# Kernel optimization log

Measured on AMD Instinct MI355X. Metric: run time of the kernel, lower is better.

## Reference

```python
import jax, jax.numpy as jnp
import numpy as np

DIM = 512
HEADS = 8
DIM_HEAD = 64
LANDMARKS = 256  # dim // 2
PINV_ITERS = 6
KERNEL = 33  # residual conv kernel
NUM_LAYERS = 2
NUM_CLASSES = 2


def layernorm(x, g, b, eps=1e-5):
    mu = x.mean(-1, keepdims=True)
    var = ((x - mu) ** 2).mean(-1, keepdims=True)
    return (x - mu) * jax.lax.rsqrt(var + eps) * g + b


def moore_penrose_pinv(x, iters=PINV_ITERS):
    # x: (b, h, m, m); scaling uses GLOBAL max over all batch/heads (torch.max)
    abs_x = jnp.abs(x)
    col = abs_x.sum(-1).max()
    row = abs_x.sum(-2).max()
    z = jnp.swapaxes(x, -1, -2) / (col * row)
    I = jnp.eye(x.shape[-1], dtype=x.dtype)
    for _ in range(iters):
        xz = x @ z
        z = 0.25 * z @ (13. * I - xz @ (15. * I - xz @ (7. * I - xz)))
    return z


def nystrom_attention(x, w_qkv, w_out, b_out, conv_w):
    # x: (b, n, dim)
    b, n, _ = x.shape
    m = LANDMARKS
    pad = (m - n % m) % m
    if pad:
        x = jnp.pad(x, ((0, 0), (pad, 0), (0, 0)))  # pad at FRONT
    nf = n + pad
    qkv = x @ w_qkv  # (b, nf, 3*h*dh)
    qkv = qkv.reshape(b, nf, 3, HEADS, DIM_HEAD)
    q = jnp.transpose(qkv[:, :, 0], (0, 2, 1, 3)) * (DIM_HEAD ** -0.5)  # (b,h,nf,dh)
    k = jnp.transpose(qkv[:, :, 1], (0, 2, 1, 3))
    v = jnp.transpose(qkv[:, :, 2], (0, 2, 1, 3))
    l = nf // m
    q_l = q.reshape(b, HEADS, m, l, DIM_HEAD).mean(3)  # (b,h,m,dh)
    k_l = k.reshape(b, HEADS, m, l, DIM_HEAD).mean(3)
    sim1 = jnp.einsum('bhid,bhjd->bhij', q, k_l)      # (b,h,nf,m)
    sim2 = jnp.einsum('bhid,bhjd->bhij', q_l, k_l)    # (b,h,m,m)
    sim3 = jnp.einsum('bhid,bhjd->bhij', q_l, k)      # (b,h,m,nf)
    attn1 = jax.nn.softmax(sim1, axis=-1)
    attn2 = jax.nn.softmax(sim2, axis=-1)
    attn3 = jax.nn.softmax(sim3, axis=-1)
    attn2_inv = moore_penrose_pinv(attn2)
    out = (attn1 @ attn2_inv) @ (attn3 @ v)  # (b,h,nf,dh)
    # residual depthwise conv over sequence dim, per head (Conv2d groups=heads)
    res = jax.lax.conv_general_dilated(
        v, conv_w, window_strides=(1, 1), padding=((KERNEL // 2, KERNEL // 2), (0, 0)),
        dimension_numbers=('NCHW', 'OIHW', 'NCHW'), feature_group_count=HEADS)
    out = out + res
    out = jnp.transpose(out, (0, 2, 1, 3)).reshape(b, nf, HEADS * DIM_HEAD)
    out = out @ w_out + b_out
    return out[:, -n:]


def setup_inputs() -> dict:
    key = jax.random.key(0)
    ks = jax.random.split(key, 16)
    B, N = 2, 8191
    s = 0.02
    inp = {
        'h': jax.random.normal(ks[0], (B, N, 1024), jnp.float32),
        'w1': jax.random.normal(ks[1], (1024, DIM), jnp.float32) * s,
        'b1': jnp.zeros((DIM,), jnp.float32),
        'cls_token': jax.random.normal(ks[2], (1, 1, DIM), jnp.float32),
        'ln_g': jnp.ones((NUM_LAYERS, DIM), jnp.float32),
        'ln_b': jnp.zeros((NUM_LAYERS, DIM), jnp.float32),
        'w_qkv': jax.random.normal(ks[3], (NUM_LAYERS, DIM, 3 * HEADS * DIM_HEAD), jnp.float32) * s,
        'w_out': jax.random.normal(ks[4], (NUM_LAYERS, HEADS * DIM_HEAD, DIM), jnp.float32) * s,
        'b_out': jnp.zeros((NUM_LAYERS, DIM), jnp.float32),
        'conv_w': jax.random.normal(ks[5], (NUM_LAYERS, HEADS, 1, KERNEL, 1), jnp.float32) * s,
        'fn_g': jnp.ones((DIM,), jnp.float32),
        'fn_b': jnp.zeros((DIM,), jnp.float32),
        'w2': jax.random.normal(ks[6], (DIM, NUM_CLASSES), jnp.float32) * s,
        'b2': jnp.zeros((NUM_CLASSES,), jnp.float32),
    }
    return inp


def reference(h, w1, b1, cls_token, ln_g, ln_b, w_qkv, w_out, b_out, conv_w, fn_g, fn_b, w2, b2):
    x = jax.nn.relu(h @ w1 + b1)  # (B,N,512)
    B = x.shape[0]
    cls = jnp.broadcast_to(cls_token, (B, 1, DIM))
    x = jnp.concatenate([cls, x], axis=1)  # (B, N+1, 512)
    for i in range(NUM_LAYERS):
        x = x + nystrom_attention(layernorm(x, ln_g[i], ln_b[i]), w_qkv[i], w_out[i], b_out[i], conv_w[i])
    x = layernorm(x, fn_g, fn_b)[:, 0]
    logits = x @ w2 + b2
    return logits
```

## Files before the change

kernel.cpp:

```cpp
#include <hip/hip_runtime.h>
#include <hip/hip_bf16.h>

#define DIM 512
#define HEADS 8
#define DH 64
#define LM 256
#define NF 8192
#define BHN 16

typedef __attribute__((ext_vector_type(8))) short short8;
typedef __attribute__((ext_vector_type(4))) float f32x4;

__device__ __forceinline__ float bf2f(unsigned short u) {
  return __uint_as_float((unsigned)u << 16);
}
__device__ __forceinline__ unsigned short f2bf(float x) {
  unsigned u = __float_as_uint(x);
  unsigned r = u + 0x7fffu + ((u >> 16) & 1u);
  return (unsigned short)(r >> 16);
}

__device__ __forceinline__ void gl2lds16(const void* g, void* l) {
  __builtin_amdgcn_global_load_lds(
      (const __attribute__((address_space(1))) void*)g,
      (__attribute__((address_space(3))) void*)l, 16, 0, 0);
}

__device__ __forceinline__ float waveReduceSum(float v) {
#pragma unroll
  for (int o = 1; o < 64; o <<= 1) v += __shfl_xor(v, o);
  return v;
}
__device__ __forceinline__ float waveReduceMax(float v) {
#pragma unroll
  for (int o = 1; o < 64; o <<= 1) v = fmaxf(v, __shfl_xor(v, o));
  return v;
}
__device__ __forceinline__ float blockReduceSum256(float v, float* sm) {
  v = waveReduceSum(v);
  int w = threadIdx.x >> 6;
  __syncthreads();
  if ((threadIdx.x & 63) == 0) sm[w] = v;
  __syncthreads();
  return sm[0] + sm[1] + sm[2] + sm[3];
}
__device__ __forceinline__ float blockReduceMax256(float v, float* sm) {
  v = waveReduceMax(v);
  int w = threadIdx.x >> 6;
  __syncthreads();
  if ((threadIdx.x & 63) == 0) sm[w] = v;
  __syncthreads();
  return fmaxf(fmaxf(sm[0], sm[1]), fmaxf(sm[2], sm[3]));
}

__global__ __launch_bounds__(256)
void cvt_bf16(const float* __restrict__ in, unsigned short* __restrict__ out,
              long long n) {
  long long i = ((long long)blockIdx.x * 256 + threadIdx.x) * 4;
  if (i + 3 < n) {
    float4 v = *(const float4*)&in[i];
    ushort4 o;
    o.x = f2bf(v.x); o.y = f2bf(v.y); o.z = f2bf(v.z); o.w = f2bf(v.w);
    *(ushort4*)&out[i] = o;
  } else {
    for (; i < n; i++) out[i] = f2bf(in[i]);
  }
}

__global__ __launch_bounds__(256)
void cvt_transpose(const float* __restrict__ in, unsigned short* __restrict__ out,
                   int Kd, int Nd) {
  __shared__ float t[32][33];
  int x = threadIdx.x & 31, y = threadIdx.x >> 5;
#pragma unroll
  for (int i = 0; i < 32; i += 8) {
    int k = blockIdx.y * 32 + y + i, n = blockIdx.x * 32 + x;
    t[y + i][x] = in[(long long)k * Nd + n];
  }
  __syncthreads();
#pragma unroll
  for (int i = 0; i < 32; i += 8) {
    int n = blockIdx.x * 32 + y + i, k = blockIdx.y * 32 + x;
    out[(long long)n * Kd + k] = f2bf(t[x][y + i]);
  }
}

__global__ __launch_bounds__(256)
void vt_transpose(const unsigned short* __restrict__ VB,
                  unsigned short* __restrict__ VT) {
  __shared__ unsigned short t[64][80];
  int bh = blockIdx.x >> 7, tile = blockIdx.x & 127;
  int n0 = tile * 64;
  int tid = threadIdx.x;
#pragma unroll
  for (int it = 0; it < 2; it++) {
    int s = it * 256 + tid;
    int nl = s >> 3, sg = s & 7;
    *(short8*)&t[nl][sg * 8] =
        *(const short8*)&VB[((long long)bh * NF + n0 + nl) * DH + sg * 8];
  }
  __syncthreads();
#pragma unroll
  for (int it = 0; it < 2; it++) {
    int s = it * 256 + tid;
    int dl = s >> 3, sg = s & 7;
    short8 v;
#pragma unroll
    for (int j = 0; j < 8; j++) ((unsigned short*)&v)[j] = t[sg * 8 + j][dl];
    *(short8*)&VT[((long long)bh * DH + dl) * NF + n0 + sg * 8] = v;
  }
}

__global__ __launch_bounds__(256) void zero_f(float* __restrict__ p, int n) {
  int i = blockIdx.x * 256 + threadIdx.x;
  if (i < n) p[i] = 0.f;
}

__global__ __launch_bounds__(256) void write_cls(const float* __restrict__ cls,
                                                 float* __restrict__ X) {
  int t = blockIdx.x * 256 + threadIdx.x;
  int b = t >> 9, c = t & 511;
  X[(long long)b * NF * DIM + c] = cls[c];
}

#define MG_RELU 1
#define MG_ADDC 2
#define MG_BIAS 4
__global__ __launch_bounds__(256)
void gemm_mfma(const unsigned short* __restrict__ A,
               const unsigned short* __restrict__ B,
               const float* __restrict__ bias, float* __restrict__ C,
               unsigned short* __restrict__ qkv, unsigned short* __restrict__ vbuf,
               int M, int N, int K, int flags, int remap) {
  __shared__ short8 smem[1024];
  short8 (*Als)[64] = (short8 (*)[64])smem;
  short8 (*Bls)[64] = (short8 (*)[64])(smem + 512);
  const int tid = threadIdx.x;
  const int lane = tid & 63, wave = tid >> 6;
  const int wm = wave >> 1, wn = wave & 1;
  const int m0 = blockIdx.y * 128, n0 = blockIdx.x * 128;
  const int r16 = lane & 15, quad = lane >> 4;
  const unsigned short* pa0 = A + (long long)(m0 + 32 * wave + r16) * K + quad * 8;
  const unsigned short* pa1 = A + (long long)(m0 + 32 * wave + 16 + r16) * K + quad * 8;
  const unsigned short* pb0 = B + (long long)(n0 + 32 * wave + r16) * K + quad * 8;
  const unsigned short* pb1 = B + (long long)(n0 + 32 * wave + 16 + r16) * K + quad * 8;
  f32x4 acc[4][4] = {};
  for (int k0 = 0; k0 < K; k0 += 32) {
    gl2lds16(pa0, &Als[2 * wave][0]);
    gl2lds16(pa1, &Als[2 * wave + 1][0]);
    gl2lds16(pb0, &Bls[2 * wave][0]);
    gl2lds16(pb1, &Bls[2 * wave + 1][0]);
    pa0 += 32; pa1 += 32; pb0 += 32; pb1 += 32;
    __syncthreads();
    short8 af[4], bfr[4];
#pragma unroll
    for (int mt = 0; mt < 4; mt++) af[mt] = Als[wm * 4 + mt][lane];
#pragma unroll
    for (int nt = 0; nt < 4; nt++) bfr[nt] = Bls[wn * 4 + nt][lane];
#pragma unroll
    for (int mt = 0; mt < 4; mt++)
#pragma unroll
      for (int nt = 0; nt < 4; nt++)
        acc[mt][nt] = __builtin_amdgcn_mfma_f32_16x16x32_bf16(
            af[mt], bfr[nt], acc[mt][nt], 0, 0, 0);
    __syncthreads();
  }
  if (remap == 2) {
    unsigned short (*Ep)[32][64] = (unsigned short (*)[32][64])smem;
    int gn_base = n0 + wn * 64;
    int s = gn_base >> 9, hh = (gn_base >> 6) & 7;
    float scale = (s == 0) ? 0.125f : 1.f;
    unsigned short* basep =
        (s == 0) ? qkv : (s == 1) ? qkv + (long long)BHN * NF * DH : vbuf;
#pragma unroll
    for (int half = 0; half < 2; half++) {
      __builtin_amdgcn_s_waitcnt(0);
#pragma unroll
      for (int mt = half * 2; mt < half * 2 + 2; mt++)
#pragma unroll
        for (int nt = 0; nt < 4; nt++)
#pragma unroll
          for (int r = 0; r < 4; r++)
            Ep[wave][(mt & 1) * 16 + quad * 4 + r][nt * 16 + r16] =
                f2bf(acc[mt][nt][r] * scale);
      __builtin_amdgcn_s_waitcnt(0);
#pragma unroll
      for (int it = 0; it < 4; it++) {
        int idx = it * 64 + lane;
        int m_l = idx >> 3, sg = idx & 7;
        int gm = m0 + wm * 64 + half * 32 + m_l;
        int b = gm >> 13, n = gm & (NF - 1);
        int bh = b * HEADS + hh;
        short8 v = *(short8*)&Ep[wave][m_l][sg * 8];
        *(short8*)&basep[((long long)bh * NF + n) * DH + sg * 8] = v;
      }
    }
  } else {
#pragma unroll
    for (int mt = 0; mt < 4; mt++) {
#pragma unroll
      for (int nt = 0; nt < 4; nt++) {
#pragma unroll
        for (int r = 0; r < 4; r++) {
          int gm = m0 + wm * 64 + mt * 16 + quad * 4 + r;
          int gn = n0 + wn * 64 + nt * 16 + r16;
          if (gm >= M) continue;
          float v = acc[mt][nt][r];
          if (flags & MG_BIAS) v += bias[gn];
          long long idx;
          if (remap == 1) {
            int b = gm / 8191;
            int n = gm - b * 8191;
            idx = ((long long)(b * NF + 1 + n)) * DIM + gn;
          } else {
            idx = (long long)gm * N + gn;
          }
          if (flags & MG_ADDC) v += C[idx];
          if (flags & MG_RELU) v = fmaxf(v, 0.f);
          C[idx] = v;
        }
      }
    }
  }
}

__global__ __launch_bounds__(256)
void flash_attn1(const unsigned short* __restrict__ QB,
                 const unsigned short* __restrict__ KLB,
                 const unsigned short* __restrict__ WmB,
                 const unsigned short* __restrict__ XNC,
                 unsigned short* __restrict__ XNB2) {
  __shared__ unsigned short Plds[4][16][136];
  const int bh = blockIdx.y, b = bh >> 3, hh = bh & 7;
  const int tid = threadIdx.x, lane = tid & 63, wave = tid >> 6;
  const int r16 = lane & 15, quad = lane >> 4;
  const int m0w = blockIdx.x * 64 + wave * 16;
  const unsigned short* Aq = QB + (long long)bh * NF * DH;
  const unsigned short* Bk = KLB + (long long)bh * LM * DH;
  short8 af[2];
#pragma unroll
  for (int kc = 0; kc < 2; kc++)
    af[kc] = *(const short8*)&Aq[(long long)(m0w + r16) * DH + kc * 32 + quad * 8];
  f32x4 S[16] = {};
  __builtin_amdgcn_s_setprio(1);
#pragma unroll
  for (int nt = 0; nt < 16; nt++) {
#pragma unroll
    for (int kc = 0; kc < 2; kc++) {
      short8 bb = *(const short8*)&Bk[(long long)(nt * 16 + r16) * DH + kc * 32 + quad * 8];
      S[nt] = __builtin_amdgcn_mfma_f32_16x16x32_bf16(af[kc], bb, S[nt], 0, 0, 0);
    }
  }
  __builtin_amdgcn_s_setprio(0);
  float inv[4];
#pragma unroll
  for (int r = 0; r < 4; r++) {
    float m_ = S[0][r];
#pragma unroll
    for (int nt = 1; nt < 16; nt++) m_ = fmaxf(m_, S[nt][r]);
#pragma unroll
    for (int o = 1; o < 16; o <<= 1) m_ = fmaxf(m_, __shfl_xor(m_, o));
    float s_ = 0.f;
#pragma unroll
    for (int nt = 0; nt < 16; nt++) {
      float e = __expf(S[nt][r] - m_);
      S[nt][r] = e;
      s_ += e;
    }
#pragma unroll
    for (int o = 1; o < 16; o <<= 1) s_ += __shfl_xor(s_, o);
    inv[r] = 1.f / s_;
  }
  f32x4 O[4] = {};
#pragma unroll
  for (int half = 0; half < 2; half++) {
#pragma unroll
    for (int nt = 0; nt < 8; nt++)
#pragma unroll
      for (int r = 0; r < 4; r++)
        Plds[wave][quad * 4 + r][nt * 16 + r16] =
            f2bf(S[half * 8 + nt][r] * inv[r]);
    __builtin_amdgcn_s_waitcnt(0);
    __builtin_amdgcn_s_setprio(1);
#pragma unroll
    for (int kc = 0; kc < 4; kc++) {
      short8 a = *(short8*)&Plds[wave][r16][kc * 32 + quad * 8];
#pragma unroll
      for (int nt2 = 0; nt2 < 4; nt2++) {
        short8 bb = *(const short8*)&WmB[((long long)bh * DH + nt2 * 16 + r16) * LM +
                                         half * 128 + kc * 32 + quad * 8];
        O[nt2] = __builtin_amdgcn_mfma_f32_16x16x32_bf16(a, bb, O[nt2], 0, 0, 0);
      }
    }
    __builtin_amdgcn_s_setprio(0);
  }
#pragma unroll
  for (int nt2 = 0; nt2 < 4; nt2++)
#pragma unroll
    for (int r = 0; r < 4; r++) {
      int row = m0w + quad * 4 + r;
      int d = nt2 * 16 + r16;
      long long gi = ((long long)(b * NF + row)) * DIM + hh * DH + d;
      XNB2[gi] = f2bf(O[nt2][r] + bf2f(XNC[gi]));
    }
}

__global__ __launch_bounds__(256)
void flash_attn3(const unsigned short* __restrict__ QLB,
                 const unsigned short* __restrict__ KB,
                 const unsigned short* __restrict__ VT,
                 float* __restrict__ Opart, float* __restrict__ Mpart,
                 float* __restrict__ Lpart) {
  __shared__ unsigned short Plds[4][16][136];
  const int bh = blockIdx.z, ks = blockIdx.y;
  const int tid = threadIdx.x, lane = tid & 63, wave = tid >> 6;
  const int r16 = lane & 15, quad = lane >> 4;
  const int m0w = blockIdx.x * 64 + wave * 16;
  const unsigned short* Aq = QLB + (long long)bh * LM * DH;
  const unsigned short* Bk = KB + (long long)bh * NF * DH;
  const unsigned short* Vt = VT + (long long)bh * DH * NF;
  short8 af[2];
#pragma unroll
  for (int kc = 0; kc < 2; kc++)
    af[kc] = *(const short8*)&Aq[(long long)(m0w + r16) * DH + kc * 32 + quad * 8];
  f32x4 O[4] = {};
  float rm[4] = {-1e30f, -1e30f, -1e30f, -1e30f};
  float rl[4] = {};
  for (int t = 0; t < 4; t++) {
    int kv0 = ks * 512 + t * 128;
    f32x4 S[8] = {};
    __builtin_amdgcn_s_setprio(1);
#pragma unroll
    for (int nt = 0; nt < 8; nt++) {
#pragma unroll
      for (int kc = 0; kc < 2; kc++) {
        short8 bb = *(const short8*)&Bk[(long long)(kv0 + nt * 16 + r16) * DH +
                                        kc * 32 + quad * 8];
        S[nt] = __builtin_amdgcn_mfma_f32_16x16x32_bf16(af[kc], bb, S[nt], 0, 0, 0);
      }
    }
    __builtin_amdgcn_s_setprio(0);
#pragma unroll
    for (int r = 0; r < 4; r++) {
      float mt = S[0][r];
#pragma unroll
      for (int nt = 1; nt < 8; nt++) mt = fmaxf(mt, S[nt][r]);
#pragma unroll
      for (int o = 1; o < 16; o <<= 1) mt = fmaxf(mt, __shfl_xor(mt, o));
      float nm = fmaxf(rm[r], mt);
      float al = __expf(rm[r] - nm);
      rm[r] = nm;
      float s_ = 0.f;
#pragma unroll
      for (int nt = 0; nt < 8; nt++) {
        float e = __expf(S[nt][r] - nm);
        S[nt][r] = e;
        s_ += e;
      }
#pragma unroll
      for (int o = 1; o < 16; o <<= 1) s_ += __shfl_xor(s_, o);
      rl[r] = rl[r] * al + s_;
#pragma unroll
      for (int nt2 = 0; nt2 < 4; nt2++) O[nt2][r] *= al;
    }
#pragma unroll
    for (int nt = 0; nt < 8; nt++)
#pragma unroll
      for (int r = 0; r < 4; r++)
        Plds[wave][quad * 4 + r][nt * 16 + r16] = f2bf(S[nt][r]);
    __builtin_amdgcn_s_waitcnt(0);
    __builtin_amdgcn_s_setprio(1);
#pragma unroll
    for (int kc2 = 0; kc2 < 4; kc2++) {
      short8 a = *(short8*)&Plds[wave][r16][kc2 * 32 + quad * 8];
#pragma unroll
      for (int nt2 = 0; nt2 < 4; nt2++) {
        short8 bb = *(const short8*)&Vt[(long long)(nt2 * 16 + r16) * NF + kv0 +
                                        kc2 * 32 + quad * 8];
        O[nt2] = __builtin_amdgcn_mfma_f32_16x16x32_bf16(a, bb, O[nt2], 0, 0, 0);
      }
    }
    __builtin_amdgcn_s_setprio(0);
  }
  float* Ob = Opart + (((long long)ks * BHN + bh) * LM) * DH;
#pragma unroll
  for (int nt2 = 0; nt2 < 4; nt2++)
#pragma unroll
    for (int r = 0; r < 4; r++) {
      int row = m0w + quad * 4 + r;
      Ob[(long long)row * DH + nt2 * 16 + r16] = O[nt2][r];
    }
  if (r16 == 0) {
#pragma unroll
    for (int r = 0; r < 4; r++) {
      int row = m0w + quad * 4 + r;
      Mpart[((long long)ks * BHN + bh) * LM + row] = rm[r];
      Lpart[((long long)ks * BHN + bh) * LM + row] = rl[r];
    }
  }
}

__global__ __launch_bounds__(256)
void attn3_merge(const float* __restrict__ Opart, const float* __restrict__ Mpart,
                 const float* __restrict__ Lpart, float* __restrict__ O3) {
  int idx = blockIdx.x * 256 + threadIdx.x;
  int bh = idx >> 14, rem = idx & 16383;
  int row = rem >> 6, d = rem & 63;
  float mg = -1e30f;
#pragma unroll
  for (int c = 0; c < 16; c++)
    mg = fmaxf(mg, Mpart[((long long)c * BHN + bh) * LM + row]);
  float L = 0.f, acc = 0.f;
#pragma unroll
  for (int c = 0; c < 16; c++) {
    float e = __expf(Mpart[((long long)c * BHN + bh) * LM + row] - mg);
    L += Lpart[((long long)c * BHN + bh) * LM + row] * e;
    acc += Opart[(((long long)c * BHN + bh) * LM + row) * DH + d] * e;
  }
  O3[((long long)bh * LM + row) * DH + d] = acc / L;
}

__global__ __launch_bounds__(256)
void zinit(const float* __restrict__ a2, const unsigned* __restrict__ red,
           unsigned short* __restrict__ zn, unsigned short* __restrict__ zt) {
  float scale = 1.0f / __uint_as_float(red[1]);
  long long idx = (long long)blockIdx.x * 256 + threadIdx.x;
  int bh = (int)(idx >> 16);
  int ij = (int)(idx & 65535);
  int i = ij >> 8, j = ij & 255;
  zn[idx] = f2bf(a2[((long long)bh << 16) + (j << 8) + i] * scale);
  zt[idx] = f2bf(a2[idx] * scale);
}

#define PV_CN 1
#define PV_CT 2
#define PV_CF 4
#define PV_ID 8
__global__ __launch_bounds__(256)
void pinv_bf(const unsigned short* __restrict__ An,
             const unsigned short* __restrict__ Bt,
             unsigned short* __restrict__ Cn, unsigned short* __restrict__ Ct,
             float* __restrict__ Cf, float alpha, float ident, float beta,
             int flags) {
  __shared__ unsigned short Als[32][256];
  __shared__ unsigned short Bls[32][256];
  const int batch = blockIdx.z;
  An += (long long)batch * 65536;
  Bt += (long long)batch * 65536;
  const int tid = threadIdx.x, lane = tid & 63, wave = tid >> 6;
  const int wm2 = wave >> 1, wn2 = wave & 1;
  const int m0 = blockIdx.y * 32, n0 = blockIdx.x * 32;
  const int r16 = lane & 15, quad = lane >> 4;
#pragma unroll
  for (int j = 0; j < 4; j++) {
    int g = (j * 4 + wave) * 64 + lane;
    int row = g >> 5, plog = (g & 31) ^ (row & 7);
    gl2lds16(An + ((m0 + row) << 8) + plog * 8,
             (char*)Als + (j * 4 + wave) * 1024);
    gl2lds16(Bt + ((n0 + row) << 8) + plog * 8,
             (char*)Bls + (j * 4 + wave) * 1024);
  }
  __syncthreads();
  f32x4 acc = {};
  const int arow = wm2 * 16 + r16, brow = wn2 * 16 + r16;
#pragma unroll
  for (int kk = 0; kk < 8; kk++) {
    short8 af = *(const short8*)((const char*)Als + arow * 512 +
                                 ((kk * 4 + quad) ^ (arow & 7)) * 16);
    short8 bfr = *(const short8*)((const char*)Bls + brow * 512 +
                                  ((kk * 4 + quad) ^ (brow & 7)) * 16);
    acc = __builtin_amdgcn_mfma_f32_16x16x32_bf16(af, bfr, acc, 0, 0, 0);
  }
  long long cb = (long long)batch * 65536;
  int ncol = n0 + wn2 * 16 + r16;
  float vals[4];
#pragma unroll
  for (int r = 0; r < 4; r++) {
    int mrow = wm2 * 16 + quad * 4 + r;
    float v = beta * acc[r];
    if (flags & PV_ID) {
      unsigned short a = *(const unsigned short*)(
          (const char*)Als + mrow * 512 +
          (((ncol >> 3) ^ (mrow & 7)) * 16) + (ncol & 7) * 2);
      v += ident * bf2f(a);
    }
    vals[r] = v * alpha;
    int gm = m0 + mrow;
    if (flags & PV_CN) Cn[cb + ((long long)gm << 8) + ncol] = f2bf(vals[r]);
    if (flags & PV_CF) Cf[cb + ((long long)gm << 8) + ncol] = vals[r];
  }
  if (flags & PV_CT) {
    ushort4 o;
    o.x = f2bf(vals[0]); o.y = f2bf(vals[1]);
    o.z = f2bf(vals[2]); o.w = f2bf(vals[3]);
    *(ushort4*)&Ct[cb + ((long long)ncol << 8) + m0 + wm2 * 16 + quad * 4] = o;
  }
}

#define BG_BIDENT 16
__global__ __launch_bounds__(256)
void bgemm(const float* __restrict__ A, const float* __restrict__ B,
           float* __restrict__ C, int M, int N, int K,
           long long sA, long long sB, long long sC,
           float alpha, float ident, int flags) {
  const int batch = blockIdx.z;
  A += (long long)batch * sA;
  B += (long long)batch * sB;
  float* Cb = C + (long long)batch * sC;
  __shared__ float As[16][68];
  __shared__ float Bs[16][68];
  const int tid = threadIdx.x;
  const int tx = tid & 15, ty = tid >> 4;
  const int m0 = blockIdx.y * 64, n0 = blockIdx.x * 64;
  float acc[4][4] = {};
  for (int k0 = 0; k0 < K; k0 += 16) {
    {
      int k = tid & 15;
      int mBase = tid >> 4;
#pragma unroll
      for (int i = 0; i < 4; i++) {
        int m = mBase + i * 16;
        int gm = m0 + m;
        As[k][m] = (gm < M) ? A[(long long)gm * K + (k0 + k)] : 0.f;
      }
    }
    {
      int n = tid & 63;
      int kBase = tid >> 6;
#pragma unroll
      for (int i = 0; i < 4; i++) {
        int k = kBase + i * 4;
        int gn = n0 + n;
        float vb = (gn < N) ? B[(long long)(k0 + k) * N + gn] : 0.f;
        if (flags & BG_BIDENT) vb = ident * ((k0 + k) == gn ? 1.f : 0.f) - vb;
        Bs[k][n] = vb;
      }
    }
    __syncthreads();
#pragma unroll
    for (int k = 0; k < 16; k++) {
      float a[4], b[4];
#pragma unroll
      for (int i = 0; i < 4; i++) a[i] = As[k][ty * 4 + i];
#pragma unroll
      for (int j = 0; j < 4; j++) b[j] = Bs[k][tx * 4 + j];
#pragma unroll
      for (int i = 0; i < 4; i++)
#pragma unroll
        for (int j = 0; j < 4; j++) acc[i][j] = fmaf(a[i], b[j], acc[i][j]);
    }
    __syncthreads();
  }
#pragma unroll
  for (int i = 0; i < 4; i++) {
    int gm = m0 + ty * 4 + i;
    if (gm >= M) continue;
#pragma unroll
    for (int j = 0; j < 4; j++) {
      int gn = n0 + tx * 4 + j;
      if (gn >= N) continue;
      Cb[(long long)gm * N + gn] = alpha * acc[i][j];
    }
  }
}

__global__ __launch_bounds__(256)
void wm_gemm(const float* __restrict__ Z, const float* __restrict__ O3,
             unsigned short* __restrict__ WmT) {
  const int batch = blockIdx.y;
  const int m0 = blockIdx.x * 64;
  const float* A = Z + (long long)batch * 65536;
  const float* B = O3 + (long long)batch * LM * DH;
  __shared__ float As[16][68];
  __shared__ float Bs[16][68];
  const int tid = threadIdx.x, tx = tid & 15, ty = tid >> 4;
  float acc[4][4] = {};
  for (int k0 = 0; k0 < 256; k0 += 16) {
    {
      int k = tid & 15, mB = tid >> 4;
#pragma unroll
      for (int i = 0; i < 4; i++) {
        int m = mB + i * 16;
        As[k][m] = A[(long long)(m0 + m) * 256 + k0 + k];
      }
    }
    {
      int n = tid & 63, kB = tid >> 6;
#pragma unroll
      for (int i = 0; i < 4; i++) {
        int k = kB + i * 4;
        Bs[k][n] = B[(long long)(k0 + k) * DH + n];
      }
    }
    __syncthreads();
#pragma unroll
    for (int k = 0; k < 16; k++) {
      float a[4], b[4];
#pragma unroll
      for (int i = 0; i < 4; i++) a[i] = As[k][ty * 4 + i];
#pragma unroll
      for (int j = 0; j < 4; j++) b[j] = Bs[k][tx * 4 + j];
#pragma unroll
      for (int i = 0; i < 4; i++)
#pragma unroll
        for (int j = 0; j < 4; j++) acc[i][j] = fmaf(a[i], b[j], acc[i][j]);
    }
    __syncthreads();
  }
#pragma unroll
  for (int i = 0; i < 4; i++)
#pragma unroll
    for (int j = 0; j < 4; j++)
      WmT[((long long)batch * DH + tx * 4 + j) * LM + m0 + ty * 4 + i] =
          f2bf(acc[i][j]);
}

__global__ __launch_bounds__(256)
void layernorm_rows_bf16(const float* __restrict__ X, const float* __restrict__ g,
                         const float* __restrict__ bt,
                         unsigned short* __restrict__ Y) {
  __shared__ float sm[4];
  long long r = blockIdx.x;
  const float* x = X + r * DIM;
  int t = threadIdx.x;
  float v0 = x[t], v1 = x[t + 256];
  float mu = blockReduceSum256(v0 + v1, sm) * (1.f / DIM);
  float d0 = v0 - mu, d1 = v1 - mu;
  float var = blockReduceSum256(d0 * d0 + d1 * d1, sm) * (1.f / DIM);
  float rs = 1.0f / sqrtf(var + 1e-5f);
  unsigned short* y = Y + r * DIM;
  y[t] = f2bf(d0 * rs * g[t] + bt[t]);
  y[t + 256] = f2bf(d1 * rs * g[t + 256] + bt[t + 256]);
}

__global__ __launch_bounds__(64)
void landmarks_k(const unsigned short* __restrict__ q,
                 const unsigned short* __restrict__ k,
                 float* __restrict__ ql, float* __restrict__ kl,
                 unsigned short* __restrict__ qlb,
                 unsigned short* __restrict__ klb) {
  int bh = blockIdx.x >> 8, i = blockIdx.x & 255, d = threadIdx.x;
  long long base = ((long long)bh * NF + i * 32) * DH + d;
  float sq = 0.f, sk = 0.f;
#pragma unroll 4
  for (int l = 0; l < 32; l++) {
    sq += bf2f(q[base + (long long)l * DH]);
    sk += bf2f(k[base + (long long)l * DH]);
  }
  long long o = ((long long)bh * LM + i) * DH + d;
  float mq = sq * (1.f / 32.f), mk = sk * (1.f / 32.f);
  ql[o] = mq; kl[o] = mk;
  qlb[o] = f2bf(mq); klb[o] = f2bf(mk);
}

__global__ __launch_bounds__(256)
void sim2_softmax(const float* __restrict__ ql, const float* __restrict__ kl,
                  float* __restrict__ a2, unsigned short* __restrict__ a2b) {
  __shared__ float qs[64];
  __shared__ float sm[4];
  int bh = blockIdx.x >> 8, i = blockIdx.x & 255, t = threadIdx.x;
  if (t < 64) qs[t] = ql[((long long)bh * LM + i) * DH + t];
  __syncthreads();
  const float* krow = kl + (long long)bh * LM * DH + (long long)t * DH;
  float s = 0.f;
#pragma unroll
  for (int d = 0; d < 64; d++) s += qs[d] * krow[d];
  float m = blockReduceMax256(s, sm);
  float e = expf(s - m);
  float sum = blockReduceSum256(e, sm);
  long long off = ((long long)bh * LM + i) * LM + t;
  float v = e / sum;
  a2[off] = v;
  a2b[off] = f2bf(v);
}

__global__ __launch_bounds__(256)
void pinv_reduce(const float* __restrict__ a2, unsigned* __restrict__ red) {
  __shared__ float sm[4];
  int bh = blockIdx.x, t = threadIdx.x;
  const float* A = a2 + (long long)bh * LM * LM;
  float cs = 0.f;
  for (int i = 0; i < 256; i++) cs += fabsf(A[i * 256 + t]);
  float cm = blockReduceMax256(cs, sm);
  if (t == 0) atomicMax(&red[1], __float_as_uint(cm));
}

__global__ __launch_bounds__(256)
void conv_res_bf16(const unsigned short* __restrict__ vt,
                   const float* __restrict__ cw,
                   unsigned short* __restrict__ out) {
  int bh = blockIdx.x >> 6, tile = blockIdx.x & 63;
  int b = bh >> 3, hh = bh & 7;
  int t = threadIdx.x;
  int d = t & 63, pg = t >> 6;
  float wr[33];
#pragma unroll
  for (int kk = 0; kk < 33; kk++) wr[kk] = cw[hh * 33 + kk];
  const unsigned short* src = &vt[((long long)bh * DH + d) * NF];
  int base = tile * 128 + pg * 32;
  int n0 = base - 16;
  float win[64];
#pragma unroll
  for (int jj = 0; jj < 8; jj++) {
    int c = n0 + jj * 8;
    if (c >= 0 && c + 7 < NF) {
      short8 v = *(const short8*)&src[c];
#pragma unroll
      for (int j = 0; j < 8; j++)
        win[jj * 8 + j] = bf2f((unsigned short)v[j]);
    } else {
#pragma unroll
      for (int j = 0; j < 8; j++) {
        int nn = c + j;
        win[jj * 8 + j] = (nn >= 0 && nn < NF) ? bf2f(src[nn]) : 0.f;
      }
    }
  }
  unsigned short* dst = &out[((long long)(b * NF + base)) * DIM + hh * DH + d];
#pragma unroll
  for (int p = 0; p < 32; p++) {
    float s = 0.f;
#pragma unroll
    for (int kk = 0; kk < 33; kk++) s = fmaf(wr[kk], win[p + kk], s);
    dst[(long long)p * DIM] = f2bf(s);
  }
}

__global__ __launch_bounds__(256)
void final_head(const float* __restrict__ X, const float* __restrict__ g,
                const float* __restrict__ bt, const float* __restrict__ w2,
                const float* __restrict__ b2, float* __restrict__ out) {
  __shared__ float sm[4];
  int b = blockIdx.x, t = threadIdx.x;
  const float* row = X + (long long)b * NF * DIM;
  float v0 = row[t], v1 = row[t + 256];
  float mu = blockReduceSum256(v0 + v1, sm) * (1.f / DIM);
  float d0 = v0 - mu, d1 = v1 - mu;
  float var = blockReduceSum256(d0 * d0 + d1 * d1, sm) * (1.f / DIM);
  float rs = 1.0f / sqrtf(var + 1e-5f);
  float y0 = d0 * rs * g[t] + bt[t];
  float y1 = d1 * rs * g[t + 256] + bt[t + 256];
  float l0 = y0 * w2[t * 2 + 0] + y1 * w2[(t + 256) * 2 + 0];
  float l1 = y0 * w2[t * 2 + 1] + y1 * w2[(t + 256) * 2 + 1];
  l0 = blockReduceSum256(l0, sm);
  l1 = blockReduceSum256(l1, sm);
  if (t == 0) {
    out[b * 2 + 0] = l0 + b2[0];
    out[b * 2 + 1] = l1 + b2[1];
  }
}

extern "C" void kernel_launch(void* const* d_in, const int* in_sizes, int n_in,
                              void* d_out, int out_size, void* d_ws,
                              size_t ws_size, hipStream_t stream) {
  const float* h      = (const float*)d_in[0];
  const float* w1     = (const float*)d_in[1];
  const float* b1     = (const float*)d_in[2];
  const float* cls    = (const float*)d_in[3];
  const float* ln_g   = (const float*)d_in[4];
  const float* ln_b   = (const float*)d_in[5];
  const float* w_qkv  = (const float*)d_in[6];
  const float* w_out  = (const float*)d_in[7];
  const float* b_out  = (const float*)d_in[8];
  const float* conv_w = (const float*)d_in[9];
  const float* fn_g   = (const float*)d_in[10];
  const float* fn_b   = (const float*)d_in[11];
  const float* w2     = (const float*)d_in[12];
  const float* b2     = (const float*)d_in[13];

  float* ws = (float*)d_ws;
  const long long XSZ = (long long)2 * NF * DIM;
  const long long QSZ = (long long)BHN * NF * DH;
  float* X  = ws;
  unsigned short* STAGE = (unsigned short*)(X + XSZ);
  unsigned short* HB   = STAGE;
  unsigned short* XNB1 = STAGE;
  unsigned short* XNB2 = STAGE;
  unsigned short* VB   = STAGE + XSZ;
  unsigned short* XNC  = STAGE + XSZ;
  unsigned short* QB = STAGE + 2 * XSZ;
  unsigned short* KB = QB + QSZ;
  unsigned short* VT = KB + QSZ;
  float* QL = (float*)(VT + QSZ);
  float* KL = QL + 262144;
  unsigned short* QLB = (unsigned short*)(KL + 262144);
  unsigned short* KLB = QLB + 262144;
  float* A2 = (float*)(KLB + 262144);
  float* ZA = A2 + 1048576;
  float* ZB = ZA + 1048576;
  float* P  = ZB + 1048576;
  float* T1 = P + 1048576;
  float* T2 = T1 + 1048576;
  float* Mpart = T2 + 1048576;
  float* Lpart = Mpart + 65536;
  float* O3 = Lpart + 65536;
  unsigned short* WmB = (unsigned short*)(O3 + 262144);
  unsigned* RED = (unsigned*)(WmB + 262144);
  unsigned short* WT = (unsigned short*)(RED + 4);
  unsigned short* W1T = WT;
  unsigned short* WQ0 = W1T + 524288;
  unsigned short* WQ1 = WQ0 + 786432;
  unsigned short* WO0 = WQ1 + 786432;
  unsigned short* WO1 = WO0 + 262144;

  unsigned short* A2B = VB;
  float* Opart = (float*)VB;
  unsigned short* Zan = (unsigned short*)P;
  unsigned short* Zat = Zan + 1048576;
  unsigned short* Zbn = (unsigned short*)ZB;
  unsigned short* Zbt = Zbn + 1048576;
  unsigned short* Pn  = (unsigned short*)T1;
  unsigned short* Pt  = Pn + 1048576;
  unsigned short* T1t = (unsigned short*)T2;
  unsigned short* T2t = T1t + 1048576;

  write_cls<<<4, 256, 0, stream>>>(cls, X);
  cvt_bf16<<<16382, 256, 0, stream>>>(h, HB, (long long)16382 * 1024);
  cvt_transpose<<<dim3(512 / 32, 1024 / 32), 256, 0, stream>>>(w1, W1T, 1024, 512);
  cvt_transpose<<<dim3(1536 / 32, 512 / 32), 256, 0, stream>>>(w_qkv, WQ0, 512, 1536);
  cvt_transpose<<<dim3(1536 / 32, 512 / 32), 256, 0, stream>>>(
      w_qkv + (long long)DIM * 1536, WQ1, 512, 1536);
  cvt_transpose<<<dim3(512 / 32, 512 / 32), 256, 0, stream>>>(w_out, WO0, 512, 512);
  cvt_transpose<<<dim3(512 / 32, 512 / 32), 256, 0, stream>>>(
      w_out + (long long)DIM * DIM, WO1, 512, 512);
  gemm_mfma<<<dim3(4, 128), 256, 0, stream>>>(HB, W1T, b1, X, nullptr, nullptr,
                                              16382, 512, 1024, MG_RELU | MG_BIAS, 1);

  for (int L = 0; L < 2; L++) {
    layernorm_rows_bf16<<<2 * NF, 256, 0, stream>>>(X, ln_g + L * DIM,
                                                    ln_b + L * DIM, XNB1);
    gemm_mfma<<<dim3(12, 128), 256, 0, stream>>>(XNB1, L ? WQ1 : WQ0, nullptr,
                                                 nullptr, QB, VB, 16384, 1536,
                                                 512, 0, 2);
    vt_transpose<<<BHN * 128, 256, 0, stream>>>(VB, VT);

    landmarks_k<<<BHN * LM, 64, 0, stream>>>(QB, KB, QL, KL, QLB, KLB);
    sim2_softmax<<<BHN * LM, 256, 0, stream>>>(QL, KL, A2, A2B);
    zero_f<<<1, 256, 0, stream>>>((float*)RED, 4);
    pinv_reduce<<<BHN, 256, 0, stream>>>(A2, RED);
    zinit<<<4096, 256, 0, stream>>>(A2, RED, Zan, Zat);
    for (int it = 0; it < 5; it++) {
      const unsigned short* zcn = (it & 1) ? Zbn : Zan;
      const unsigned short* zct = (it & 1) ? Zbt : Zat;
      unsigned short* znn = (it & 1) ? Zan : Zbn;
      unsigned short* znt = (it & 1) ? Zat : Zbt;
      pinv_bf<<<dim3(8, 8, BHN), 256, 0, stream>>>(
          A2B, zct, Pn, Pt, nullptr, 1.f, 0.f, 1.f, PV_CN | PV_CT);
      pinv_bf<<<dim3(8, 8, BHN), 256, 0, stream>>>(
          Pn, Pt, nullptr, T1t, nullptr, 1.f, 7.f, -1.f, PV_CT | PV_ID);
      pinv_bf<<<dim3(8, 8, BHN), 256, 0, stream>>>(
          Pn, T1t, nullptr, T2t, nullptr, 1.f, 15.f, -1.f, PV_CT | PV_ID);
      if (it < 4)
        pinv_bf<<<dim3(8, 8, BHN), 256, 0, stream>>>(
            zcn, T2t, znn, znt, nullptr, 0.25f, 13.f, -1.f,
            PV_CN | PV_CT | PV_ID);
      else
        pinv_bf<<<dim3(8, 8, BHN), 256, 0, stream>>>(
            zcn, T2t, nullptr, nullptr, ZB, 0.25f, 13.f, -1.f, PV_CF | PV_ID);
    }
    bgemm<<<dim3(4, 4, BHN), 256, 0, stream>>>(A2, ZB, P, 256, 256, 256,
                                               65536, 65536, 65536, 1.f, 0.f, 0);
    bgemm<<<dim3(4, 4, BHN), 256, 0, stream>>>(P, P, T1, 256, 256, 256,
                                               65536, 65536, 65536, 1.f, 7.f,
                                               BG_BIDENT);
    bgemm<<<dim3(4, 4, BHN), 256, 0, stream>>>(P, T1, T2, 256, 256, 256,
                                               65536, 65536, 65536, 1.f, 15.f,
                                               BG_BIDENT);
    bgemm<<<dim3(4, 4, BHN), 256, 0, stream>>>(ZB, T2, ZA, 256, 256, 256,
                                               65536, 65536, 65536, 0.25f,
                                               13.f, BG_BIDENT);

    flash_attn3<<<dim3(4, 16, BHN), 256, 0, stream>>>(QLB, KB, VT, Opart, Mpart,
                                                      Lpart);
    attn3_merge<<<1024, 256, 0, stream>>>(Opart, Mpart, Lpart, O3);

    wm_gemm<<<dim3(4, BHN), 256, 0, stream>>>(ZA, O3, WmB);

    conv_res_bf16<<<BHN * 64, 256, 0, stream>>>(VT, conv_w + L * 264, XNC);

    flash_attn1<<<dim3(128, BHN), 256, 0, stream>>>(QB, KLB, WmB, XNC, XNB2);

    gemm_mfma<<<dim3(4, 128), 256, 0, stream>>>(XNB2, L ? WO1 : WO0,
                                                b_out + L * DIM, X, nullptr,
                                                nullptr, 16384, 512, 512,
                                                MG_ADDC | MG_BIAS, 0);
  }
  final_head<<<2, 256, 0, stream>>>(X, fn_g, fn_b, w2, b2, (float*)d_out);
}
```

Baseline: 1.464 ms.

## Use online softmax in attn1, lds-only fences, occupancy hints, memset

flash_attn1 now computes its softmax online over two 128-column tiles, so only 8 score accumulators are live instead of 16, and normalization is deferred to the output store. Full s_waitcnt(0) barriers before LDS reads are replaced with an lgkmcnt-only wait plus a scheduling barrier, so outstanding global loads no longer stall those points. Both flash kernels get a min-blocks launch bound of 8 to push register usage down for higher occupancy. The zero_f kernel launch is replaced with hipMemsetAsync. The occupancy bound may force register spills, and online rescaling adds a few extra exponentials.

```diff
diff --git a/kernel.cpp b/kernel.cpp
--- a/kernel.cpp
+++ b/kernel.cpp
@@ -24,6 +24,11 @@
   __builtin_amdgcn_global_load_lds(
       (const __attribute__((address_space(1))) void*)g,
       (__attribute__((address_space(3))) void*)l, 16, 0, 0);
+}
+
+__device__ __forceinline__ void lds_fence() {
+  asm volatile("s_waitcnt lgkmcnt(0)" ::: "memory");
+  __builtin_amdgcn_sched_barrier(0);
 }
 
 __device__ __forceinline__ float waveReduceSum(float v) {
@@ -109,11 +114,6 @@
     for (int j = 0; j < 8; j++) ((unsigned short*)&v)[j] = t[sg * 8 + j][dl];
     *(short8*)&VT[((long long)bh * DH + dl) * NF + n0 + sg * 8] = v;
   }
-}
-
-__global__ __launch_bounds__(256) void zero_f(float* __restrict__ p, int n) {
-  int i = blockIdx.x * 256 + threadIdx.x;
-  if (i < n) p[i] = 0.f;
 }
 
 __global__ __launch_bounds__(256) void write_cls(const float* __restrict__ cls,
@@ -174,7 +174,7 @@
         (s == 0) ? qkv : (s == 1) ? qkv + (long long)BHN * NF * DH : vbuf;
 #pragma unroll
     for (int half = 0; half < 2; half++) {
-      __builtin_amdgcn_s_waitcnt(0);
+      lds_fence();
 #pragma unroll
       for (int mt = half * 2; mt < half * 2 + 2; mt++)
 #pragma unroll
@@ -183,7 +183,7 @@
           for (int r = 0; r < 4; r++)
             Ep[wave][(mt & 1) * 16 + quad * 4 + r][nt * 16 + r16] =
                 f2bf(acc[mt][nt][r] * scale);
-      __builtin_amdgcn_s_waitcnt(0);
+      lds_fence();
 #pragma unroll
       for (int it = 0; it < 4; it++) {
         int idx = it * 64 + lane;
@@ -224,7 +224,7 @@
   }
 }
 
-__global__ __launch_bounds__(256)
+__global__ __launch_bounds__(256, 8)
 void flash_attn1(const unsigned short* __restrict__ QB,
                  const unsigned short* __restrict__ KLB,
                  const unsigned short* __restrict__ WmB,
@@ -237,63 +237,74 @@
   const int m0w = blockIdx.x * 64 + wave * 16;
   const unsigned short* Aq = QB + (long long)bh * NF * DH;
   const unsigned short* Bk = KLB + (long long)bh * LM * DH;
+  const unsigned short* Wm = WmB + (long long)bh * DH * LM;
   short8 af[2];
 #pragma unroll
   for (int kc = 0; kc < 2; kc++)
     af[kc] = *(const short8*)&Aq[(long long)(m0w + r16) * DH + kc * 32 + quad * 8];
-  f32x4 S[16] = {};
-  __builtin_amdgcn_s_setprio(1);
-#pragma unroll
-  for (int nt = 0; nt < 16; nt++) {
-#pragma unroll
-    for (int kc = 0; kc < 2; kc++) {
-      short8 bb = *(const short8*)&Bk[(long long)(nt * 16 + r16) * DH + kc * 32 + quad * 8];
-      S[nt] = __builtin_amdgcn_mfma_f32_16x16x32_bf16(af[kc], bb, S[nt], 0, 0, 0);
-    }
-  }
-  __builtin_amdgcn_s_setprio(0);
-  float inv[4];
-#pragma unroll
-  for (int r = 0; r < 4; r++) {
-    float m_ = S[0][r];
-#pragma unroll
-    for (int nt = 1; nt < 16; nt++) m_ = fmaxf(m_, S[nt][r]);
-#pragma unroll
-    for (int o = 1; o < 16; o <<= 1) m_ = fmaxf(m_, __shfl_xor(m_, o));
-    float s_ = 0.f;
-#pragma unroll
-    for (int nt = 0; nt < 16; nt++) {
-      float e = __expf(S[nt][r] - m_);
-      S[nt][r] = e;
-      s_ += e;
-    }
-#pragma unroll
-    for (int o = 1; o < 16; o <<= 1) s_ += __shfl_xor(s_, o);
-    inv[r] = 1.f / s_;
-  }
   f32x4 O[4] = {};
-#pragma unroll
-  for (int half = 0; half < 2; half++) {
+  float rm[4] = {-1e30f, -1e30f, -1e30f, -1e30f};
+  float rl[4] = {};
+#pragma unroll
+  for (int t = 0; t < 2; t++) {
+    int c0 = t * 128;
+    f32x4 S[8] = {};
+    __builtin_amdgcn_s_setprio(1);
+#pragma unroll
+    for (int nt = 0; nt < 8; nt++) {
+#pragma unroll
+      for (int kc = 0; kc < 2; kc++) {
+        short8 bb = *(const short8*)&Bk[(long long)(c0 + nt * 16 + r16) * DH +
+                                        kc * 32 + quad * 8];
+        S[nt] = __builtin_amdgcn_mfma_f32_16x16x32_bf16(af[kc], bb, S[nt], 0, 0, 0);
+      }
+    }
+    __builtin_amdgcn_s_setprio(0);
+#pragma unroll
+    for (int r = 0; r < 4; r++) {
+      float mt = S[0][r];
+#pragma unroll
+      for (int nt = 1; nt < 8; nt++) mt = fmaxf(mt, S[nt][r]);
+#pragma unroll
+      for (int o = 1; o < 16; o <<= 1) mt = fmaxf(mt, __shfl_xor(mt, o));
+      float nm = fmaxf(rm[r], mt);
+      float al = __expf(rm[r] - nm);
+      rm[r] = nm;
+      float s_ = 0.f;
+#pragma unroll
+      for (int nt = 0; nt < 8; nt++) {
+        float e = __expf(S[nt][r] - nm);
+        S[nt][r] = e;
+        s_ += e;
+      }
+#pragma unroll
+      for (int o = 1; o < 16; o <<= 1) s_ += __shfl_xor(s_, o);
+      rl[r] = rl[r] * al + s_;
+#pragma unroll
+      for (int nt2 = 0; nt2 < 4; nt2++) O[nt2][r] *= al;
+    }
 #pragma unroll
     for (int nt = 0; nt < 8; nt++)
 #pragma unroll
       for (int r = 0; r < 4; r++)
-        Plds[wave][quad * 4 + r][nt * 16 + r16] =
-            f2bf(S[half * 8 + nt][r] * inv[r]);
-    __builtin_amdgcn_s_waitcnt(0);
+        Plds[wave][quad * 4 + r][nt * 16 + r16] = f2bf(S[nt][r]);
+    lds_fence();
     __builtin_amdgcn_s_setprio(1);
 #pragma unroll
     for (int kc = 0; kc < 4; kc++) {
       short8 a = *(short8*)&Plds[wave][r16][kc * 32 + quad * 8];
 #pragma unroll
       for (int nt2 = 0; nt2 < 4; nt2++) {
-        short8 bb = *(const short8*)&WmB[((long long)bh * DH + nt2 * 16 + r16) * LM +
-                                         half * 128 + kc * 32 + quad * 8];
+        short8 bb = *(const short8*)&Wm[(long long)(nt2 * 16 + r16) * LM + c0 +
+                                        kc * 32 + quad * 8];
         O[nt2] = __builtin_amdgcn_mfma_f32_16x16x32_bf16(a, bb, O[nt2], 0, 0, 0);
       }
     }
     __builtin_amdgcn_s_setprio(0);
   }
+  float invl[4];
+#pragma unroll
+  for (int r = 0; r < 4; r++) invl[r] = 1.f / rl[r];
 #pragma unroll
   for (int nt2 = 0; nt2 < 4; nt2++)
 #pragma unroll
@@ -301,11 +312,11 @@
       int row = m0w + quad * 4 + r;
       int d = nt2 * 16 + r16;
       long long gi = ((long long)(b * NF + row)) * DIM + hh * DH + d;
-      XNB2[gi] = f2bf(O[nt2][r] + bf2f(XNC[gi]));
-    }
-}
-
-__global__ __launch_bounds__(256)
+      XNB2[gi] = f2bf(O[nt2][r] * invl[r] + bf2f(XNC[gi]));
+    }
+}
+
+__global__ __launch_bounds__(256, 8)
 void flash_attn3(const unsigned short* __restrict__ QLB,
                  const unsigned short* __restrict__ KB,
                  const unsigned short* __restrict__ VT,
@@ -368,7 +379,7 @@
 #pragma unroll
       for (int r = 0; r < 4; r++)
         Plds[wave][quad * 4 + r][nt * 16 + r16] = f2bf(S[nt][r]);
-    __builtin_amdgcn_s_waitcnt(0);
+    lds_fence();
     __builtin_amdgcn_s_setprio(1);
 #pragma unroll
     for (int kc2 = 0; kc2 < 4; kc2++) {
@@ -836,7 +847,7 @@
 
     landmarks_k<<<BHN * LM, 64, 0, stream>>>(QB, KB, QL, KL, QLB, KLB);
     sim2_softmax<<<BHN * LM, 256, 0, stream>>>(QL, KL, A2, A2B);
-    zero_f<<<1, 256, 0, stream>>>((float*)RED, 4);
+    hipMemsetAsync(RED, 0, 16, stream);
     pinv_reduce<<<BHN, 256, 0, stream>>>(A2, RED);
     zinit<<<4096, 256, 0, stream>>>(A2, RED, Zan, Zat);
     for (int it = 0; it < 5; it++) {
```

New measurement: 1.725 ms. 1.18x slower.
